# Optimization experiments

Measured on AMD Instinct MI355X. Metric: run time of the kernel, lower is better.

Reference implementation:

```python
import jax, jax.numpy as jnp
import numpy as np


def _gen_grid(rotations, size):
    # Replicates _Volume.VolumeGenGrid(U^T, grid): rotate normalized voxel coords.
    # grid[b,d,h,w,:] = R^T @ [x_w, y_h, z_d], components ordered (x,y,z) for grid_sample.
    c = jnp.linspace(-1.0, 1.0, size, dtype=jnp.float32)
    zz, yy, xx = jnp.meshgrid(c, c, c, indexing='ij')      # [S,S,S] each (d,h,w)
    base = jnp.stack([xx, yy, zz], axis=-1)                 # [S,S,S,3]
    UT = jnp.swapaxes(rotations, 1, 2)                      # [B,3,3]
    return jnp.einsum('bij,dhwj->bdhwi', UT, base)          # [B,S,S,S,3]


def _grid_sample_3d(vol, grid):
    # Trilinear grid_sample, padding_mode='zeros', align_corners=False (torch default).
    B, C, D, H, W = vol.shape
    x = (grid[..., 0] + 1.0) * W * 0.5 - 0.5
    y = (grid[..., 1] + 1.0) * H * 0.5 - 0.5
    z = (grid[..., 2] + 1.0) * D * 0.5 - 0.5
    x0 = jnp.floor(x); y0 = jnp.floor(y); z0 = jnp.floor(z)
    tx = x - x0; ty = y - y0; tz = z - z0
    vol_flat = vol.reshape(B, C, D * H * W)
    out = jnp.zeros(vol.shape, dtype=vol.dtype)
    for dz in (0, 1):
        for dy in (0, 1):
            for dx in (0, 1):
                xi = x0 + dx; yi = y0 + dy; zi = z0 + dz
                w = (jnp.where(dx, tx, 1.0 - tx)
                     * jnp.where(dy, ty, 1.0 - ty)
                     * jnp.where(dz, tz, 1.0 - tz))
                valid = ((xi >= 0) & (xi < W) & (yi >= 0) & (yi < H)
                         & (zi >= 0) & (zi < D))
                xi_c = jnp.clip(xi, 0, W - 1).astype(jnp.int32)
                yi_c = jnp.clip(yi, 0, H - 1).astype(jnp.int32)
                zi_c = jnp.clip(zi, 0, D - 1).astype(jnp.int32)
                lin = (zi_c * H + yi_c) * W + xi_c              # [B,S,S,S]
                lin = lin.reshape(B, 1, -1)
                g = jnp.take_along_axis(vol_flat, jnp.broadcast_to(lin, (B, C, lin.shape[-1])), axis=2)
                wm = (w * valid.astype(vol.dtype)).reshape(B, 1, -1)
                out = out + (g * wm).reshape(vol.shape)
    return out


def setup_inputs() -> dict:
    key = jax.random.key(0)
    k1, k2 = jax.random.split(key)
    B, C, S = 8, 16, 64
    input_volume = jax.random.normal(k1, (B, C, S, S, S), dtype=jnp.float32)
    A = jax.random.normal(k2, (B, 3, 3), dtype=jnp.float32)
    Q, _ = jnp.linalg.qr(A)                                  # orthonormal rotations
    rotations = Q.astype(jnp.float32)
    return {"input_volume": input_volume, "rotations": rotations}


def reference(input_volume, rotations):
    size = input_volume.shape[2]
    grid = _gen_grid(rotations, size)
    return _grid_sample_3d(input_volume, grid)
```

## Files before the change

### kernel.cpp

```cpp
#include <hip/hip_runtime.h>


#define S 64
#define SP (S * S * S)
#define CCH 16
#define BB 8

#define TW 16
#define TH 8
#define TD 8
#define NT 512
#define PPT 2
#define CAP 8192
#define MAXIT 16

__global__ __launch_bounds__(NT, 4) void vol_rot_tiled(
    const float* __restrict__ vol,
    const float* __restrict__ rot,
    float* __restrict__ out)
{
    __shared__ float smem[CAP + 2];

    const int tid = threadIdx.x;

    const int wg = (blockIdx.x & 7) * (BB * 256 / 8) + (blockIdx.x >> 3);
    const int t  = wg & 255;
    const int b  = wg >> 8;
    const int w0 = (t & 3) * TW;
    const int h0 = ((t >> 2) & 7) * TH;
    const int d0 = (t >> 5) * TD;

    const float* R = rot + b * 9;
    const float R00 = R[0], R01 = R[1], R02 = R[2];
    const float R10 = R[3], R11 = R[4], R12 = R[5];
    const float R20 = R[6], R21 = R[7], R22 = R[8];

    const float st = 2.0f / 63.0f;

    float xmn = 1e30f, xmx = -1e30f;
    float ymn = 1e30f, ymx = -1e30f;
    float zmn = 1e30f, zmx = -1e30f;
#pragma unroll
    for (int k = 0; k < 8; ++k) {
        const float xb = -1.0f + (float)(w0 + ((k & 1) ? (TW - 1) : 0)) * st;
        const float yb = -1.0f + (float)(h0 + ((k & 2) ? (TH - 1) : 0)) * st;
        const float zb = -1.0f + (float)(d0 + ((k & 4) ? (TD - 1) : 0)) * st;
        const float gx = R00 * xb + R10 * yb + R20 * zb;
        const float gy = R01 * xb + R11 * yb + R21 * zb;
        const float gz = R02 * xb + R12 * yb + R22 * zb;
        const float vx = (gx + 1.0f) * 32.0f - 0.5f;
        const float vy = (gy + 1.0f) * 32.0f - 0.5f;
        const float vz = (gz + 1.0f) * 32.0f - 0.5f;
        xmn = fminf(xmn, vx); xmx = fmaxf(xmx, vx);
        ymn = fminf(ymn, vy); ymx = fmaxf(ymx, vy);
        zmn = fminf(zmn, vz); zmx = fmaxf(zmx, vz);
    }
    const int rx0 = (int)floorf(xmn);
    const int ry0 = (int)floorf(ymn);
    const int rz0 = (int)floorf(zmn);
    int ex = (int)floorf(xmx) + 2 - rx0;
    int ey = (int)floorf(ymx) + 2 - ry0;
    int ez = (int)floorf(zmx) + 2 - rz0;
    if (ex * ey * ez > CAP) ez = CAP / (ex * ey);

    const int plane = ex * ey;
    const int rsz   = plane * ez;
    const int nit   = (rsz + NT - 1) >> 9;
    const float invp = 1.0f / (float)plane;
    const float inve = 1.0f / (float)ex;

    int voff[MAXIT];
    unsigned mask = 0;
#define STAGE_ADDR(i)                                                         \
    if (nit > (i)) {                                                          \
        const int r  = tid + (i) * NT;                                        \
        const int rz = (int)(((float)r + 0.5f) * invp);                       \
        const int rm = r - rz * plane;                                        \
        const int ry = (int)(((float)rm + 0.5f) * inve);                      \
        const int rx = rm - ry * ex;                                          \
        const int gx = rx0 + rx, gy = ry0 + ry, gz = rz0 + rz;                \
        const bool valid = ((unsigned)gx < 64u) & ((unsigned)gy < 64u)        \
                         & ((unsigned)gz < 64u);                              \
        const int gxc = min(max(gx, 0), 63);                                  \
        const int gyc = min(max(gy, 0), 63);                                  \
        const int gzc = min(max(gz, 0), 63);                                  \
        voff[i] = (((((gzc << 6) + gyc) << 6) + gxc) << 2);                   \
        mask |= ((unsigned)valid) << (i);                                     \
    }
    STAGE_ADDR(0)  STAGE_ADDR(1)  STAGE_ADDR(2)  STAGE_ADDR(3)
    STAGE_ADDR(4)  STAGE_ADDR(5)  STAGE_ADDR(6)  STAGE_ADDR(7)
    STAGE_ADDR(8)  STAGE_ADDR(9)  STAGE_ADDR(10) STAGE_ADDR(11)
    STAGE_ADDR(12) STAGE_ADDR(13) STAGE_ADDR(14) STAGE_ADDR(15)
#undef STAGE_ADDR

    int   obase[PPT];
    int   ospat[PPT];
    float wgt[PPT][8];
#pragma unroll
    for (int p = 0; p < PPT; ++p) {
        const int idx = tid + p * NT;
        const int pw = idx & 15, ph = (idx >> 4) & 7, pd = idx >> 7;
        const float xb = -1.0f + (float)(w0 + pw) * st;
        const float yb = -1.0f + (float)(h0 + ph) * st;
        const float zb = -1.0f + (float)(d0 + pd) * st;
        const float gx = R00 * xb + R10 * yb + R20 * zb;
        const float gy = R01 * xb + R11 * yb + R21 * zb;
        const float gz = R02 * xb + R12 * yb + R22 * zb;
        const float vx = (gx + 1.0f) * 32.0f - 0.5f;
        const float vy = (gy + 1.0f) * 32.0f - 0.5f;
        const float vz = (gz + 1.0f) * 32.0f - 0.5f;
        const float fx = floorf(vx), fy = floorf(vy), fz = floorf(vz);
        const float tx = vx - fx, ty = vy - fy, tz = vz - fz;
        int lx = (int)fx - rx0, ly = (int)fy - ry0, lz = (int)fz - rz0;
        lx = min(max(lx, 0), ex - 2);
        ly = min(max(ly, 0), ey - 2);
        lz = min(max(lz, 0), ez - 2);
        obase[p] = ((lz * ey + ly) * ex + lx) * 4;
        ospat[p] = ((d0 + pd) * 64 + (h0 + ph)) * 64 + (w0 + pw);
        const float ux = 1.0f - tx, uy = 1.0f - ty, uz = 1.0f - tz;
        wgt[p][0] = uz * uy * ux; wgt[p][1] = uz * uy * tx;
        wgt[p][2] = uz * ty * ux; wgt[p][3] = uz * ty * tx;
        wgt[p][4] = tz * uy * ux; wgt[p][5] = tz * uy * tx;
        wgt[p][6] = tz * ty * ux; wgt[p][7] = tz * ty * tx;
    }

    const char* smemb = (const char*)smem;
    const int dy4 = ex * 4;
    const int dz4 = plane * 4;
    const float* volb = vol + (size_t)b * CCH * SP;
    float*       outb = out + (size_t)b * CCH * SP;

    float vals[MAXIT];
#define PREFETCH(i, vc)                                                       \
    if (nit > (i)) vals[i] = *(const float*)((vc) + voff[i]);
#define LDS_WRITE(i)                                                          \
    if (nit > (i))                                                            \
        smem[tid + (i) * NT] = ((mask >> (i)) & 1u) ? vals[i] : 0.0f;

    {
        const char* vc = (const char*)volb;
        PREFETCH(0, vc)  PREFETCH(1, vc)  PREFETCH(2, vc)  PREFETCH(3, vc)
        PREFETCH(4, vc)  PREFETCH(5, vc)  PREFETCH(6, vc)  PREFETCH(7, vc)
        PREFETCH(8, vc)  PREFETCH(9, vc)  PREFETCH(10, vc) PREFETCH(11, vc)
        PREFETCH(12, vc) PREFETCH(13, vc) PREFETCH(14, vc) PREFETCH(15, vc)
    }

    for (int c = 0; c < CCH; ++c) {
        __syncthreads();
        LDS_WRITE(0)  LDS_WRITE(1)  LDS_WRITE(2)  LDS_WRITE(3)
        LDS_WRITE(4)  LDS_WRITE(5)  LDS_WRITE(6)  LDS_WRITE(7)
        LDS_WRITE(8)  LDS_WRITE(9)  LDS_WRITE(10) LDS_WRITE(11)
        LDS_WRITE(12) LDS_WRITE(13) LDS_WRITE(14) LDS_WRITE(15)
        __syncthreads();

        if (c + 1 < CCH) {
            const char* vc = (const char*)(volb + (c + 1) * SP);
            PREFETCH(0, vc)  PREFETCH(1, vc)  PREFETCH(2, vc)  PREFETCH(3, vc)
            PREFETCH(4, vc)  PREFETCH(5, vc)  PREFETCH(6, vc)  PREFETCH(7, vc)
            PREFETCH(8, vc)  PREFETCH(9, vc)  PREFETCH(10, vc) PREFETCH(11, vc)
            PREFETCH(12, vc) PREFETCH(13, vc) PREFETCH(14, vc) PREFETCH(15, vc)
        }

#pragma unroll
        for (int p = 0; p < PPT; ++p) {
            const char* pb = smemb + obase[p];
            const float v000 = *(const float*)(pb);
            const float v001 = *(const float*)(pb + 4);
            const float v010 = *(const float*)(pb + dy4);
            const float v011 = *(const float*)(pb + dy4 + 4);
            const float v100 = *(const float*)(pb + dz4);
            const float v101 = *(const float*)(pb + dz4 + 4);
            const float v110 = *(const float*)(pb + dz4 + dy4);
            const float v111 = *(const float*)(pb + dz4 + dy4 + 4);
            const float acc = wgt[p][0] * v000 + wgt[p][1] * v001
                            + wgt[p][2] * v010 + wgt[p][3] * v011
                            + wgt[p][4] * v100 + wgt[p][5] * v101
                            + wgt[p][6] * v110 + wgt[p][7] * v111;
            outb[c * SP + ospat[p]] = acc;
        }
    }
#undef PREFETCH
#undef LDS_WRITE
}

extern "C" void kernel_launch(void* const* d_in, const int* in_sizes, int n_in,
                              void* d_out, int out_size, void* d_ws, size_t ws_size,
                              hipStream_t stream) {
    const float* vol = (const float*)d_in[0];
    const float* rot = (const float*)d_in[1];
    float* out = (float*)d_out;

    vol_rot_tiled<<<dim3(BB * 256), dim3(NT), 0, stream>>>(vol, rot, out);
}
```

Baseline: 384.4 us.

## Use 8x8x8 tiles with double-buffered LDS and two-channel register prefetch

Shrinks the output tile from 16x8x8 to 8x8x8, so each thread produces one voxel per channel and there are twice as many workgroups. Splits shared memory into two halves so one channel is written to LDS while the previous one is sampled. This drops to a single barrier per channel, with global prefetch issued two channels ahead. Smaller tiles raise the halo overhead per output voxel, and there is a truncation risk if a rotated footprint exceeds the 4608-float half buffer.

```diff
diff --git a/kernel.cpp b/kernel.cpp
--- a/kernel.cpp
+++ b/kernel.cpp
@@ -6,29 +6,27 @@
 #define CCH 16
 #define BB 8
 
-#define TW 16
-#define TH 8
-#define TD 8
+#define TS 8
 #define NT 512
-#define PPT 2
-#define CAP 8192
-#define MAXIT 16
-
-__global__ __launch_bounds__(NT, 4) void vol_rot_tiled(
+#define TPB 512
+#define HALF 4608
+#define MAXIT 9
+
+__global__ __launch_bounds__(NT, 8) void vol_rot_dbuf(
     const float* __restrict__ vol,
     const float* __restrict__ rot,
     float* __restrict__ out)
 {
-    __shared__ float smem[CAP + 2];
+    __shared__ float smem[2 * HALF];
 
     const int tid = threadIdx.x;
 
-    const int wg = (blockIdx.x & 7) * (BB * 256 / 8) + (blockIdx.x >> 3);
-    const int t  = wg & 255;
-    const int b  = wg >> 8;
-    const int w0 = (t & 3) * TW;
-    const int h0 = ((t >> 2) & 7) * TH;
-    const int d0 = (t >> 5) * TD;
+    const int wg = (blockIdx.x & 7) * TPB + (blockIdx.x >> 3);
+    const int t  = wg & (TPB - 1);
+    const int b  = wg >> 9;
+    const int w0 = (t & 7) << 3;
+    const int h0 = ((t >> 3) & 7) << 3;
+    const int d0 = (t >> 6) << 3;
 
     const float* R = rot + b * 9;
     const float R00 = R[0], R01 = R[1], R02 = R[2];
@@ -42,9 +40,9 @@
     float zmn = 1e30f, zmx = -1e30f;
 #pragma unroll
     for (int k = 0; k < 8; ++k) {
-        const float xb = -1.0f + (float)(w0 + ((k & 1) ? (TW - 1) : 0)) * st;
-        const float yb = -1.0f + (float)(h0 + ((k & 2) ? (TH - 1) : 0)) * st;
-        const float zb = -1.0f + (float)(d0 + ((k & 4) ? (TD - 1) : 0)) * st;
+        const float xb = -1.0f + (float)(w0 + ((k & 1) ? (TS - 1) : 0)) * st;
+        const float yb = -1.0f + (float)(h0 + ((k & 2) ? (TS - 1) : 0)) * st;
+        const float zb = -1.0f + (float)(d0 + ((k & 4) ? (TS - 1) : 0)) * st;
         const float gx = R00 * xb + R10 * yb + R20 * zb;
         const float gy = R01 * xb + R11 * yb + R21 * zb;
         const float gz = R02 * xb + R12 * yb + R22 * zb;
@@ -61,7 +59,7 @@
     int ex = (int)floorf(xmx) + 2 - rx0;
     int ey = (int)floorf(ymx) + 2 - ry0;
     int ez = (int)floorf(zmx) + 2 - rz0;
-    if (ex * ey * ez > CAP) ez = CAP / (ex * ey);
+    if (ex * ey * ez > HALF) ez = HALF / (ex * ey);
 
     const int plane = ex * ey;
     const int rsz   = plane * ez;
@@ -87,19 +85,15 @@
         voff[i] = (((((gzc << 6) + gyc) << 6) + gxc) << 2);                   \
         mask |= ((unsigned)valid) << (i);                                     \
     }
-    STAGE_ADDR(0)  STAGE_ADDR(1)  STAGE_ADDR(2)  STAGE_ADDR(3)
-    STAGE_ADDR(4)  STAGE_ADDR(5)  STAGE_ADDR(6)  STAGE_ADDR(7)
-    STAGE_ADDR(8)  STAGE_ADDR(9)  STAGE_ADDR(10) STAGE_ADDR(11)
-    STAGE_ADDR(12) STAGE_ADDR(13) STAGE_ADDR(14) STAGE_ADDR(15)
+    STAGE_ADDR(0) STAGE_ADDR(1) STAGE_ADDR(2) STAGE_ADDR(3) STAGE_ADDR(4)
+    STAGE_ADDR(5) STAGE_ADDR(6) STAGE_ADDR(7) STAGE_ADDR(8)
 #undef STAGE_ADDR
 
-    int   obase[PPT];
-    int   ospat[PPT];
-    float wgt[PPT][8];
-#pragma unroll
-    for (int p = 0; p < PPT; ++p) {
-        const int idx = tid + p * NT;
-        const int pw = idx & 15, ph = (idx >> 4) & 7, pd = idx >> 7;
+    int   obase;
+    int   ospat;
+    float wgt[8];
+    {
+        const int pw = tid & 7, ph = (tid >> 3) & 7, pd = tid >> 6;
         const float xb = -1.0f + (float)(w0 + pw) * st;
         const float yb = -1.0f + (float)(h0 + ph) * st;
         const float zb = -1.0f + (float)(d0 + pd) * st;
@@ -115,13 +109,13 @@
         lx = min(max(lx, 0), ex - 2);
         ly = min(max(ly, 0), ey - 2);
         lz = min(max(lz, 0), ez - 2);
-        obase[p] = ((lz * ey + ly) * ex + lx) * 4;
-        ospat[p] = ((d0 + pd) * 64 + (h0 + ph)) * 64 + (w0 + pw);
+        obase = ((lz * ey + ly) * ex + lx) * 4;
+        ospat = ((d0 + pd) * 64 + (h0 + ph)) * 64 + (w0 + pw);
         const float ux = 1.0f - tx, uy = 1.0f - ty, uz = 1.0f - tz;
-        wgt[p][0] = uz * uy * ux; wgt[p][1] = uz * uy * tx;
-        wgt[p][2] = uz * ty * ux; wgt[p][3] = uz * ty * tx;
-        wgt[p][4] = tz * uy * ux; wgt[p][5] = tz * uy * tx;
-        wgt[p][6] = tz * ty * ux; wgt[p][7] = tz * ty * tx;
+        wgt[0] = uz * uy * ux; wgt[1] = uz * uy * tx;
+        wgt[2] = uz * ty * ux; wgt[3] = uz * ty * tx;
+        wgt[4] = tz * uy * ux; wgt[5] = tz * uy * tx;
+        wgt[6] = tz * ty * ux; wgt[7] = tz * ty * tx;
     }
 
     const char* smemb = (const char*)smem;
@@ -130,57 +124,69 @@
     const float* volb = vol + (size_t)b * CCH * SP;
     float*       outb = out + (size_t)b * CCH * SP;
 
-    float vals[MAXIT];
-#define PREFETCH(i, vc)                                                       \
-    if (nit > (i)) vals[i] = *(const float*)((vc) + voff[i]);
-#define LDS_WRITE(i)                                                          \
+    float valsA[MAXIT], valsB[MAXIT];
+
+#define PREF(i, vc, ARR)                                                      \
+    if (nit > (i)) ARR[i] = *(const float*)((vc) + voff[i]);
+#define PREF9(vc, ARR)                                                        \
+    PREF(0, vc, ARR) PREF(1, vc, ARR) PREF(2, vc, ARR) PREF(3, vc, ARR)       \
+    PREF(4, vc, ARR) PREF(5, vc, ARR) PREF(6, vc, ARR) PREF(7, vc, ARR)       \
+    PREF(8, vc, ARR)
+#define WRT(i, ARR, SB)                                                       \
     if (nit > (i))                                                            \
-        smem[tid + (i) * NT] = ((mask >> (i)) & 1u) ? vals[i] : 0.0f;
+        smem[(SB) + tid + (i) * NT] = ((mask >> (i)) & 1u) ? ARR[i] : 0.0f;
+#define WRT9(ARR, SB)                                                         \
+    WRT(0, ARR, SB) WRT(1, ARR, SB) WRT(2, ARR, SB) WRT(3, ARR, SB)           \
+    WRT(4, ARR, SB) WRT(5, ARR, SB) WRT(6, ARR, SB) WRT(7, ARR, SB)           \
+    WRT(8, ARR, SB)
 
     {
         const char* vc = (const char*)volb;
-        PREFETCH(0, vc)  PREFETCH(1, vc)  PREFETCH(2, vc)  PREFETCH(3, vc)
-        PREFETCH(4, vc)  PREFETCH(5, vc)  PREFETCH(6, vc)  PREFETCH(7, vc)
-        PREFETCH(8, vc)  PREFETCH(9, vc)  PREFETCH(10, vc) PREFETCH(11, vc)
-        PREFETCH(12, vc) PREFETCH(13, vc) PREFETCH(14, vc) PREFETCH(15, vc)
-    }
-
-    for (int c = 0; c < CCH; ++c) {
-        __syncthreads();
-        LDS_WRITE(0)  LDS_WRITE(1)  LDS_WRITE(2)  LDS_WRITE(3)
-        LDS_WRITE(4)  LDS_WRITE(5)  LDS_WRITE(6)  LDS_WRITE(7)
-        LDS_WRITE(8)  LDS_WRITE(9)  LDS_WRITE(10) LDS_WRITE(11)
-        LDS_WRITE(12) LDS_WRITE(13) LDS_WRITE(14) LDS_WRITE(15)
-        __syncthreads();
-
-        if (c + 1 < CCH) {
-            const char* vc = (const char*)(volb + (c + 1) * SP);
-            PREFETCH(0, vc)  PREFETCH(1, vc)  PREFETCH(2, vc)  PREFETCH(3, vc)
-            PREFETCH(4, vc)  PREFETCH(5, vc)  PREFETCH(6, vc)  PREFETCH(7, vc)
-            PREFETCH(8, vc)  PREFETCH(9, vc)  PREFETCH(10, vc) PREFETCH(11, vc)
-            PREFETCH(12, vc) PREFETCH(13, vc) PREFETCH(14, vc) PREFETCH(15, vc)
-        }
-
-#pragma unroll
-        for (int p = 0; p < PPT; ++p) {
-            const char* pb = smemb + obase[p];
-            const float v000 = *(const float*)(pb);
-            const float v001 = *(const float*)(pb + 4);
-            const float v010 = *(const float*)(pb + dy4);
-            const float v011 = *(const float*)(pb + dy4 + 4);
-            const float v100 = *(const float*)(pb + dz4);
-            const float v101 = *(const float*)(pb + dz4 + 4);
-            const float v110 = *(const float*)(pb + dz4 + dy4);
-            const float v111 = *(const float*)(pb + dz4 + dy4 + 4);
-            const float acc = wgt[p][0] * v000 + wgt[p][1] * v001
-                            + wgt[p][2] * v010 + wgt[p][3] * v011
-                            + wgt[p][4] * v100 + wgt[p][5] * v101
-                            + wgt[p][6] * v110 + wgt[p][7] * v111;
-            outb[c * SP + ospat[p]] = acc;
-        }
-    }
-#undef PREFETCH
-#undef LDS_WRITE
+        PREF9(vc, valsA)
+    }
+    WRT9(valsA, 0)
+    {
+        const char* vc = (const char*)(volb + SP);
+        PREF9(vc, valsB)
+    }
+    __syncthreads();
+
+#define PHASE(cval, LD_ARR, WR_ARR, SB_WR, SB_SMP)                            \
+    {                                                                         \
+        const int c = (cval);                                                 \
+        if (c + 2 < CCH) {                                                    \
+            const char* vc = (const char*)(volb + (size_t)(c + 2) * SP);      \
+            PREF9(vc, LD_ARR)                                                 \
+        }                                                                     \
+        if (c + 1 < CCH) { WRT9(WR_ARR, SB_WR) }                              \
+        {                                                                     \
+            const char* pb = smemb + (SB_SMP) * 4 + obase;                    \
+            const float v000 = *(const float*)(pb);                          \
+            const float v001 = *(const float*)(pb + 4);                      \
+            const float v010 = *(const float*)(pb + dy4);                    \
+            const float v011 = *(const float*)(pb + dy4 + 4);                \
+            const float v100 = *(const float*)(pb + dz4);                    \
+            const float v101 = *(const float*)(pb + dz4 + 4);                \
+            const float v110 = *(const float*)(pb + dz4 + dy4);              \
+            const float v111 = *(const float*)(pb + dz4 + dy4 + 4);          \
+            const float acc = wgt[0] * v000 + wgt[1] * v001                   \
+                            + wgt[2] * v010 + wgt[3] * v011                   \
+                            + wgt[4] * v100 + wgt[5] * v101                   \
+                            + wgt[6] * v110 + wgt[7] * v111;                  \
+            outb[c * SP + ospat] = acc;                                       \
+        }                                                                     \
+        __syncthreads();                                                      \
+    }
+
+    for (int c2 = 0; c2 < CCH; c2 += 2) {
+        PHASE(c2,     valsA, valsB, HALF, 0)
+        PHASE(c2 + 1, valsB, valsA, 0,    HALF)
+    }
+#undef PHASE
+#undef WRT9
+#undef WRT
+#undef PREF9
+#undef PREF
 }
 
 extern "C" void kernel_launch(void* const* d_in, const int* in_sizes, int n_in,
@@ -190,5 +196,5 @@
     const float* rot = (const float*)d_in[1];
     float* out = (float*)d_out;
 
-    vol_rot_tiled<<<dim3(BB * 256), dim3(NT), 0, stream>>>(vol, rot, out);
+    vol_rot_dbuf<<<dim3(BB * TPB), dim3(NT), 0, stream>>>(vol, rot, out);
 }
```

After: 376.3 us. 2.1% less time.

## Stage volume tiles via global_load_lds direct-to-LDS and use lerp interpolation

Applied to the files above, without the earlier changes.

Global-to-register prefetch plus LDS write is replaced by direct global_load_lds into shared memory. Out-of-bounds voxels are redirected to a zero buffer. Trilinear weights are dropped in favour of nested lerps to save registers, and launch bounds rise to 6 waves per SIMD. This frees VGPRs and skips the register round trip, but gives up the software prefetch overlap of the next channel, since each channel's load now sits on the critical path between barriers.

```diff
diff --git a/kernel.cpp b/kernel.cpp
--- a/kernel.cpp
+++ b/kernel.cpp
@@ -3,6 +3,7 @@
 
 #define S 64
 #define SP (S * S * S)
+#define SPB (SP * 4)
 #define CCH 16
 #define BB 8
 
@@ -14,7 +15,12 @@
 #define CAP 8192
 #define MAXIT 16
 
-__global__ __launch_bounds__(NT, 4) void vol_rot_tiled(
+typedef const __attribute__((address_space(1))) void* gas1_t;
+typedef __attribute__((address_space(3))) void* las3_t;
+
+__device__ float g_zero[64];
+
+__global__ __launch_bounds__(NT, 6) void vol_rot_glds(
     const float* __restrict__ vol,
     const float* __restrict__ rot,
     float* __restrict__ out)
@@ -23,7 +29,7 @@
 
     const int tid = threadIdx.x;
 
-    const int wg = (blockIdx.x & 7) * (BB * 256 / 8) + (blockIdx.x >> 3);
+    const int wg = (blockIdx.x & 7) * 256 + (blockIdx.x >> 3);
     const int t  = wg & 255;
     const int b  = wg >> 8;
     const int w0 = (t & 3) * TW;
@@ -58,14 +64,15 @@
     const int rx0 = (int)floorf(xmn);
     const int ry0 = (int)floorf(ymn);
     const int rz0 = (int)floorf(zmn);
-    int ex = (int)floorf(xmx) + 2 - rx0;
-    int ey = (int)floorf(ymx) + 2 - ry0;
+    const int ex = (int)floorf(xmx) + 2 - rx0;
+    const int ey = (int)floorf(ymx) + 2 - ry0;
     int ez = (int)floorf(zmx) + 2 - rz0;
     if (ex * ey * ez > CAP) ez = CAP / (ex * ey);
 
     const int plane = ex * ey;
     const int rsz   = plane * ez;
-    const int nit   = (rsz + NT - 1) >> 9;
+    int nit = (rsz + NT - 1) >> 9;
+    nit = __builtin_amdgcn_readfirstlane(nit);
     const float invp = 1.0f / (float)plane;
     const float inve = 1.0f / (float)ex;
 
@@ -93,9 +100,9 @@
     STAGE_ADDR(12) STAGE_ADDR(13) STAGE_ADDR(14) STAGE_ADDR(15)
 #undef STAGE_ADDR
 
+    float tfx[PPT], tfy[PPT], tfz[PPT];
     int   obase[PPT];
-    int   ospat[PPT];
-    float wgt[PPT][8];
+    int   ospat0;
 #pragma unroll
     for (int p = 0; p < PPT; ++p) {
         const int idx = tid + p * NT;
@@ -110,56 +117,37 @@
         const float vy = (gy + 1.0f) * 32.0f - 0.5f;
         const float vz = (gz + 1.0f) * 32.0f - 0.5f;
         const float fx = floorf(vx), fy = floorf(vy), fz = floorf(vz);
-        const float tx = vx - fx, ty = vy - fy, tz = vz - fz;
+        tfx[p] = vx - fx; tfy[p] = vy - fy; tfz[p] = vz - fz;
         int lx = (int)fx - rx0, ly = (int)fy - ry0, lz = (int)fz - rz0;
         lx = min(max(lx, 0), ex - 2);
         ly = min(max(ly, 0), ey - 2);
         lz = min(max(lz, 0), ez - 2);
         obase[p] = ((lz * ey + ly) * ex + lx) * 4;
-        ospat[p] = ((d0 + pd) * 64 + (h0 + ph)) * 64 + (w0 + pw);
-        const float ux = 1.0f - tx, uy = 1.0f - ty, uz = 1.0f - tz;
-        wgt[p][0] = uz * uy * ux; wgt[p][1] = uz * uy * tx;
-        wgt[p][2] = uz * ty * ux; wgt[p][3] = uz * ty * tx;
-        wgt[p][4] = tz * uy * ux; wgt[p][5] = tz * uy * tx;
-        wgt[p][6] = tz * ty * ux; wgt[p][7] = tz * ty * tx;
+        if (p == 0)
+            ospat0 = ((d0 + pd) * 64 + (h0 + ph)) * 64 + (w0 + pw);
     }
 
     const char* smemb = (const char*)smem;
     const int dy4 = ex * 4;
     const int dz4 = plane * 4;
-    const float* volb = vol + (size_t)b * CCH * SP;
-    float*       outb = out + (size_t)b * CCH * SP;
+    const char*  vcb  = (const char*)vol + (size_t)b * CCH * SPB;
+    const char*  zptr = (const char*)g_zero;
+    float*       outc = out + (size_t)b * CCH * SP;
 
-    float vals[MAXIT];
-#define PREFETCH(i, vc)                                                       \
-    if (nit > (i)) vals[i] = *(const float*)((vc) + voff[i]);
-#define LDS_WRITE(i)                                                          \
-    if (nit > (i))                                                            \
-        smem[tid + (i) * NT] = ((mask >> (i)) & 1u) ? vals[i] : 0.0f;
-
-    {
-        const char* vc = (const char*)volb;
-        PREFETCH(0, vc)  PREFETCH(1, vc)  PREFETCH(2, vc)  PREFETCH(3, vc)
-        PREFETCH(4, vc)  PREFETCH(5, vc)  PREFETCH(6, vc)  PREFETCH(7, vc)
-        PREFETCH(8, vc)  PREFETCH(9, vc)  PREFETCH(10, vc) PREFETCH(11, vc)
-        PREFETCH(12, vc) PREFETCH(13, vc) PREFETCH(14, vc) PREFETCH(15, vc)
+#define GLLDS(i)                                                              \
+    if (nit > (i)) {                                                          \
+        const char* src = ((mask >> (i)) & 1u) ? (vcb + voff[i]) : zptr;      \
+        __builtin_amdgcn_global_load_lds(                                     \
+            (gas1_t)(const void*)src,                                         \
+            (las3_t)(void*)&smem[tid + (i) * NT], 4, 0, 0);                   \
     }
 
     for (int c = 0; c < CCH; ++c) {
+        GLLDS(0)  GLLDS(1)  GLLDS(2)  GLLDS(3)
+        GLLDS(4)  GLLDS(5)  GLLDS(6)  GLLDS(7)
+        GLLDS(8)  GLLDS(9)  GLLDS(10) GLLDS(11)
+        GLLDS(12) GLLDS(13) GLLDS(14) GLLDS(15)
         __syncthreads();
-        LDS_WRITE(0)  LDS_WRITE(1)  LDS_WRITE(2)  LDS_WRITE(3)
-        LDS_WRITE(4)  LDS_WRITE(5)  LDS_WRITE(6)  LDS_WRITE(7)
-        LDS_WRITE(8)  LDS_WRITE(9)  LDS_WRITE(10) LDS_WRITE(11)
-        LDS_WRITE(12) LDS_WRITE(13) LDS_WRITE(14) LDS_WRITE(15)
-        __syncthreads();
-
-        if (c + 1 < CCH) {
-            const char* vc = (const char*)(volb + (c + 1) * SP);
-            PREFETCH(0, vc)  PREFETCH(1, vc)  PREFETCH(2, vc)  PREFETCH(3, vc)
-            PREFETCH(4, vc)  PREFETCH(5, vc)  PREFETCH(6, vc)  PREFETCH(7, vc)
-            PREFETCH(8, vc)  PREFETCH(9, vc)  PREFETCH(10, vc) PREFETCH(11, vc)
-            PREFETCH(12, vc) PREFETCH(13, vc) PREFETCH(14, vc) PREFETCH(15, vc)
-        }
 
 #pragma unroll
         for (int p = 0; p < PPT; ++p) {
@@ -172,15 +160,21 @@
             const float v101 = *(const float*)(pb + dz4 + 4);
             const float v110 = *(const float*)(pb + dz4 + dy4);
             const float v111 = *(const float*)(pb + dz4 + dy4 + 4);
-            const float acc = wgt[p][0] * v000 + wgt[p][1] * v001
-                            + wgt[p][2] * v010 + wgt[p][3] * v011
-                            + wgt[p][4] * v100 + wgt[p][5] * v101
-                            + wgt[p][6] * v110 + wgt[p][7] * v111;
-            outb[c * SP + ospat[p]] = acc;
+            const float tx = tfx[p], ty = tfy[p], tz = tfz[p];
+            const float a00 = v000 + tx * (v001 - v000);
+            const float a01 = v010 + tx * (v011 - v010);
+            const float a10 = v100 + tx * (v101 - v100);
+            const float a11 = v110 + tx * (v111 - v110);
+            const float b0  = a00 + ty * (a01 - a00);
+            const float b1  = a10 + ty * (a11 - a10);
+            const float acc = b0 + tz * (b1 - b0);
+            outc[ospat0 + p * (4 * 64 * 64)] = acc;
         }
+        __syncthreads();
+        vcb  += SPB;
+        outc += SP;
     }
-#undef PREFETCH
-#undef LDS_WRITE
+#undef GLLDS
 }
 
 extern "C" void kernel_launch(void* const* d_in, const int* in_sizes, int n_in,
@@ -190,5 +184,5 @@
     const float* rot = (const float*)d_in[1];
     float* out = (float*)d_out;
 
-    vol_rot_tiled<<<dim3(BB * 256), dim3(NT), 0, stream>>>(vol, rot, out);
+    vol_rot_glds<<<dim3(BB * 256), dim3(NT), 0, stream>>>(vol, rot, out);
 }
```

New measurement: 365.9 us. 1.05x faster.
